# Kernel tuning notes

Measured on AMD Instinct MI355X. Metric: run time of the kernel, lower is better.

The kernel has to match this reference:

```python
import jax, jax.numpy as jnp
import numpy as np

B, Himg, Wimg, C = 4, 32, 32, 512
NUM_HEADS = 8
HEAD_DIM = C // NUM_HEADS          # 64
S_PATCH, L_PATCH = 4, 32           # key/value patch, query patch (l_patch == H so q has 1 patch)
SCALE = HEAD_DIM ** -0.5           # original code's self.scale is unset (bug); standard intent


def patchify(a, H, W, p):
    # a: [B, nh, N, hd] with N == H*W  ->  [B, nh, (H//p)*(W//p), p*p, hd]
    b, nh, n, hd = a.shape
    a = a.reshape(b, nh, H // p, p, W // p, p, hd)
    a = a.transpose(0, 1, 2, 4, 3, 5, 6)
    return a.reshape(b, nh, (H // p) * (W // p), p * p, hd)


def setup_inputs() -> dict:
    key = jax.random.key(0)
    ks = jax.random.split(key, 8)
    w_std = C ** -0.5  # keep qk logits O(1) so softmax is non-degenerate
    return {
        "x_s": jax.random.normal(ks[0], (B, Himg * Wimg, C), jnp.float32),
        "x_l": jax.random.normal(ks[1], (B, Himg * Wimg, C), jnp.float32),
        "Wq": jax.random.normal(ks[2], (C, C), jnp.float32) * w_std,
        "bq": jax.random.normal(ks[3], (C,), jnp.float32) * 0.01,
        "Wk": jax.random.normal(ks[4], (C, C), jnp.float32) * w_std,
        "bk": jax.random.normal(ks[5], (C,), jnp.float32) * 0.01,
        "Wv": jax.random.normal(ks[6], (C, C), jnp.float32) * w_std,
        "bv": jax.random.normal(ks[7], (C,), jnp.float32) * 0.01,
        "H": Himg,
        "W": Wimg,
    }


def reference(x_s, x_l, Wq, bq, Wk, bk, Wv, bv, H, W):
    b, n, c = x_s.shape
    # projections + split heads: [B, nh, N, hd]
    q = (x_l @ Wq + bq).reshape(b, n, NUM_HEADS, HEAD_DIM).transpose(0, 2, 1, 3)
    k = (x_s @ Wk + bk).reshape(b, n, NUM_HEADS, HEAD_DIM).transpose(0, 2, 1, 3)
    v = (x_s @ Wv + bv).reshape(b, n, NUM_HEADS, HEAD_DIM).transpose(0, 2, 1, 3)
    q_p = patchify(q, H, W, L_PATCH)   # [B, nh, 1,  L^2, hd]
    k_p = patchify(k, H, W, S_PATCH)   # [B, nh, Ps, s^2, hd]
    v_p = patchify(v, H, W, S_PATCH)   # [B, nh, Ps, s^2, hd]
    # broadcasted windowed cross-attention: [B, nh, Ps, L^2, s^2]
    attn = jnp.matmul(q_p, k_p.swapaxes(-2, -1)) * SCALE
    attn = jax.nn.softmax(attn, axis=-1)
    # dropout p=0.0 -> identity
    return jnp.matmul(attn, v_p)       # [B, nh, Ps, L^2, hd]
```

## Files before the change

### kernel.cpp

```cpp
#include <hip/hip_runtime.h>
#include <hip/hip_bf16.h>

#define NB 4
#define NH 8
#define NPX 1024
#define HD 64
#define CDIM 512
#define M_ROWS 4096
#define PS 64
#define S2 16

typedef __attribute__((ext_vector_type(8))) short bf16x8;
typedef __attribute__((ext_vector_type(4))) short bf16x4;
typedef __attribute__((ext_vector_type(4))) float f32x4;

typedef const __attribute__((address_space(1))) unsigned int* gptr_t;
typedef __attribute__((address_space(3))) unsigned int* lptr_t;

static __device__ __forceinline__ short f2bf(float f) {
    __hip_bfloat16 h = __float2bfloat16(f);
    return *reinterpret_cast<short*>(&h);
}

__global__ void convert_k(const float* __restrict__ xs, const float* __restrict__ xl,
                          const float* __restrict__ Wq, const float* __restrict__ Wk,
                          const float* __restrict__ Wv,
                          short* __restrict__ xl_bf, short* __restrict__ xs_bf,
                          short* __restrict__ WT ) {
    int i = blockIdx.x * blockDim.x + threadIdx.x;
    if (i < 524288) {
        float4 a = ((const float4*)xl)[i];
        float4 b = ((const float4*)xs)[i];
        short4 oa = make_short4(f2bf(a.x), f2bf(a.y), f2bf(a.z), f2bf(a.w));
        short4 ob = make_short4(f2bf(b.x), f2bf(b.y), f2bf(b.z), f2bf(b.w));
        ((short4*)xl_bf)[i] = oa;
        ((short4*)xs_bf)[i] = ob;
    }
    if (i < 786432) {
        int which = i >> 18;
        int j = i & 262143;
        int n = j >> 9, k = j & 511;
        const float* W = which == 0 ? Wq : (which == 1 ? Wk : Wv);
        WT[i] = f2bf(W[k * 512 + n]);
    }
}

__global__ __launch_bounds__(256, 3) void proj_gemm(
    const short* __restrict__ xl_bf, const short* __restrict__ xs_bf,
    const short* __restrict__ WT, const float* __restrict__ bq,
    const float* __restrict__ bk, const float* __restrict__ bv,
    short* __restrict__ qkv) {
    __shared__ __attribute__((aligned(16))) short A_lds[128 * 64];
    __shared__ __attribute__((aligned(16))) short B_lds[64 * 64];
    const int z = blockIdx.z;
    const int m0 = blockIdx.x * 128;
    const int n0 = blockIdx.y * 64;
    const short* A = (z == 0) ? xl_bf : xs_bf;
    const short* WTz = WT + z * 262144;
    const float* bias = (z == 0) ? bq : ((z == 1) ? bk : bv);
    short* out = qkv + (size_t)z * M_ROWS * CDIM;
    const int t = threadIdx.x, w = t >> 6, lane = t & 63;
    const int lr = lane & 15, g = lane >> 4;

    f32x4 acc[2][4] = {};
    for (int kt = 0; kt < 8; ++kt) {
        const int k0 = kt * 64;
#pragma unroll
        for (int r = 0; r < 4; ++r) {
            int c = r * 256 + t;
            int row = c >> 3, sub = c & 7;
            const short* src = A + (size_t)(m0 + row) * CDIM + k0 + ((sub ^ (row & 7)) * 8);
            __builtin_amdgcn_global_load_lds((gptr_t)src,
                (lptr_t)(A_lds + (r * 256 + w * 64) * 8), 16, 0, 0);
        }
#pragma unroll
        for (int r = 0; r < 2; ++r) {
            int c = r * 256 + t;
            int row = c >> 3, sub = c & 7;
            const short* src = WTz + (size_t)(n0 + row) * CDIM + k0 + ((sub ^ (row & 7)) * 8);
            __builtin_amdgcn_global_load_lds((gptr_t)src,
                (lptr_t)(B_lds + (r * 256 + w * 64) * 8), 16, 0, 0);
        }
        __syncthreads();
        bf16x8 afr[2][2], bfr[4][2];
#pragma unroll
        for (int mt = 0; mt < 2; ++mt)
#pragma unroll
            for (int kk = 0; kk < 2; ++kk) {
                int row = w * 32 + mt * 16 + lr;
                int slot = (kk * 4 + g) ^ (row & 7);
                afr[mt][kk] = *(const bf16x8*)(A_lds + row * 64 + slot * 8);
            }
#pragma unroll
        for (int nt = 0; nt < 4; ++nt)
#pragma unroll
            for (int kk = 0; kk < 2; ++kk) {
                int row = nt * 16 + lr;
                int slot = (kk * 4 + g) ^ (row & 7);
                bfr[nt][kk] = *(const bf16x8*)(B_lds + row * 64 + slot * 8);
            }
#pragma unroll
        for (int kk = 0; kk < 2; ++kk)
#pragma unroll
            for (int mt = 0; mt < 2; ++mt)
#pragma unroll
                for (int nt = 0; nt < 4; ++nt)
                    acc[mt][nt] = __builtin_amdgcn_mfma_f32_16x16x32_bf16(
                        afr[mt][kk], bfr[nt][kk], acc[mt][nt], 0, 0, 0);
        __syncthreads();
    }
#pragma unroll
    for (int mt = 0; mt < 2; ++mt) {
#pragma unroll
        for (int nt = 0; nt < 4; ++nt) {
            int col = n0 + nt * 16 + lr;
            float bv_ = bias[col];
            int row0 = m0 + w * 32 + mt * 16 + g * 4;
#pragma unroll
            for (int r = 0; r < 4; ++r)
                out[(size_t)(row0 + r) * CDIM + col] = f2bf(acc[mt][nt][r] + bv_);
        }
    }
}

__global__ void v_trans(const short* __restrict__ v_bf, short* __restrict__ vTp) {
    __shared__ __attribute__((aligned(16))) short lds[16 * 512];
    const int blk = blockIdx.x;
    const int b = blk >> 6, p = blk & 63;
    const int py = p >> 3, px = p & 7;
    const int t = threadIdx.x;
#pragma unroll
    for (int r = 0; r < 4; ++r) {
        int ci = r * 256 + t;
        int s = ci >> 6, c8 = (ci & 63) * 8;
        int n = py * 128 + (s >> 2) * 32 + px * 4 + (s & 3);
        *(bf16x8*)(lds + s * 512 + c8) =
            *(const bf16x8*)(v_bf + (size_t)(b * NPX + n) * CDIM + c8);
    }
    __syncthreads();
    const int h = t >> 5, d0 = (t & 31) * 2;
#pragma unroll
    for (int dd = 0; dd < 2; ++dd) {
        int d = d0 + dd;
        short tmp[16];
#pragma unroll
        for (int s = 0; s < 16; ++s) tmp[s] = lds[s * 512 + h * 64 + d];
        short* dst = vTp + ((size_t)((b * 8 + h) * PS + p) * HD + d) * S2;
        *(bf16x8*)(dst) = *(const bf16x8*)(tmp);
        *(bf16x8*)(dst + 8) = *(const bf16x8*)(tmp + 8);
    }
}

__global__ __launch_bounds__(256, 4) void attn_k(
    const short* __restrict__ q_bf, const short* __restrict__ k_bf,
    const short* __restrict__ vTp, float* __restrict__ out) {
    __shared__ __attribute__((aligned(16))) short k_lds[2][2][S2 * 64];
    __shared__ __attribute__((aligned(16))) float st_lds[4 * 16 * 68];
    const int bid = blockIdx.x;
    const int wid = ((bid & 7) << 7) | (bid >> 3);
    const int bh = wid >> 5;
    const int b = bh >> 3, h = bh & 7;
    const int rem = wid & 31;
    const int qtile = rem >> 1, pg = rem & 1;
    const int t = threadIdx.x, w = t >> 6, lane = t & 63;
    const int lr = lane & 15, g = lane >> 4;
    const int l_loc = qtile * 64 + w * 16 + lr;

    bf16x8 qfr[2];
    {
        const short* qrow = q_bf + (size_t)(b * NPX + l_loc) * CDIM + h * HD;
        qfr[0] = *(const bf16x8*)(qrow + g * 8);
        qfr[1] = *(const bf16x8*)(qrow + 32 + g * 8);
    }
    float* outbh = out + (size_t)bh * PS * NPX * HD;
    const int p0 = pg * 32;
    float* stw = st_lds + w * 1088;
    const int srow = lane >> 4, schunk = lane & 15;
    const short* vbase = vTp + ((size_t)(bh * PS) * HD + lr) * S2 + g * 4;

    const int s = t >> 4, c4 = (t & 15) * 4;
    const int swidx = (s * 64 + c4) ^ ((s & 7) << 3);
    const size_t rowbase = (size_t)(b * NPX) * CDIM + h * HD + c4;
    auto nidx = [&](int p) {
        int py = p >> 3, px = p & 7;
        return py * 128 + (s >> 2) * 32 + px * 4 + (s & 3);
    };
    short4 kreg[2];
    auto loadg = [&](int gi) {
#pragma unroll
        for (int pp = 0; pp < 2; ++pp) {
            int n = nidx(p0 + gi * 2 + pp);
            kreg[pp] = *(const short4*)(k_bf + rowbase + (size_t)n * CDIM);
        }
    };
    auto writeg = [&](int buf) {
#pragma unroll
        for (int pp = 0; pp < 2; ++pp)
            *(short4*)(&k_lds[buf][pp][swidx]) = kreg[pp];
    };
    loadg(0);
    writeg(0);
    for (int si = 0; si < 16; ++si) {
        const int buf = si & 1;
        asm volatile("s_waitcnt lgkmcnt(0)" ::: "memory");
        __builtin_amdgcn_s_barrier();
        __builtin_amdgcn_sched_barrier(0);
        if (si < 15) loadg(si + 1);
#pragma unroll
        for (int pp = 0; pp < 2; ++pp) {
            const int p = p0 + si * 2 + pp;
            const short* kb = k_lds[buf][pp];
            bf16x8 kfr0 = *(const bf16x8*)(kb + ((lr * 64 + g * 8) ^ ((lr & 7) << 3)));
            bf16x8 kfr1 = *(const bf16x8*)(kb + ((lr * 64 + 32 + g * 8) ^ ((lr & 7) << 3)));
            const short* vr = vbase + (size_t)p * HD * S2;
            bf16x4 vfr4[4];
#pragma unroll
            for (int dt = 0; dt < 4; ++dt)
                vfr4[dt] = *(const bf16x4*)(vr + dt * 16 * S2);

            f32x4 s_acc = {};
            s_acc = __builtin_amdgcn_mfma_f32_16x16x32_bf16(kfr0, qfr[0], s_acc, 0, 0, 0);
            s_acc = __builtin_amdgcn_mfma_f32_16x16x32_bf16(kfr1, qfr[1], s_acc, 0, 0, 0);
            float sv[4];
            float m = -1e30f;
#pragma unroll
            for (int r = 0; r < 4; ++r) { sv[r] = s_acc[r] * 0.125f; m = fmaxf(m, sv[r]); }
            m = fmaxf(m, __shfl_xor(m, 16));
            m = fmaxf(m, __shfl_xor(m, 32));
            float pv[4]; float sum = 0.f;
#pragma unroll
            for (int r = 0; r < 4; ++r) { pv[r] = __expf(sv[r] - m); sum += pv[r]; }
            sum += __shfl_xor(sum, 16);
            sum += __shfl_xor(sum, 32);
            float rs = 1.f / sum;
            bf16x8 pfr = { f2bf(pv[0] * rs), f2bf(pv[1] * rs), f2bf(pv[2] * rs), f2bf(pv[3] * rs),
                           0, 0, 0, 0 };
            f32x4 oacc[4];
#pragma unroll
            for (int dt = 0; dt < 4; ++dt) {
                bf16x8 vfr = { vfr4[dt][0], vfr4[dt][1], vfr4[dt][2], vfr4[dt][3], 0, 0, 0, 0 };
                f32x4 zero = {};
                oacc[dt] = __builtin_amdgcn_mfma_f32_16x16x32_bf16(vfr, pfr, zero, 0, 0, 0);
            }
#pragma unroll
            for (int dt = 0; dt < 4; ++dt)
                *(f32x4*)(stw + lr * 68 + dt * 16 + g * 4) = oacc[dt];
            float* opbase = outbh + ((size_t)p * NPX + qtile * 64 + w * 16) * HD;
#pragma unroll
            for (int u = 0; u < 4; ++u) {
                f32x4 vout = *(const f32x4*)(stw + (u * 4 + srow) * 68 + schunk * 4);
                *(f32x4*)(opbase + (size_t)(u * 4 + srow) * HD + schunk * 4) = vout;
            }
        }
        if (si < 15) writeg(buf ^ 1);
    }
}

extern "C" void kernel_launch(void* const* d_in, const int* in_sizes, int n_in,
                              void* d_out, int out_size, void* d_ws, size_t ws_size,
                              hipStream_t stream) {
    const float* x_s = (const float*)d_in[0];
    const float* x_l = (const float*)d_in[1];
    const float* Wq  = (const float*)d_in[2];
    const float* bq  = (const float*)d_in[3];
    const float* Wk  = (const float*)d_in[4];
    const float* bk  = (const float*)d_in[5];
    const float* Wv  = (const float*)d_in[6];
    const float* bv  = (const float*)d_in[7];
    float* out = (float*)d_out;
    char* ws = (char*)d_ws;

    short* xl_bf = (short*)(ws);
    short* xs_bf = (short*)(ws + 4194304);
    short* WT    = (short*)(ws + 8388608);
    short* qkv   = (short*)(ws + 9961472);
    short* q_bf = qkv;
    short* k_bf = qkv + 2097152;
    short* v_bf = qkv + 4194304;
    short* vTp  = (short*)(ws + 22544384);

    convert_k<<<3072, 256, 0, stream>>>(x_s, x_l, Wq, Wk, Wv, xl_bf, xs_bf, WT);
    proj_gemm<<<dim3(32, 8, 3), 256, 0, stream>>>(xl_bf, xs_bf, WT, bq, bk, bv, qkv);
    v_trans<<<256, 256, 0, stream>>>(v_bf, vTp);
    attn_k<<<1024, 256, 0, stream>>>(q_bf, k_bf, vTp, out);
}
```

Before: 138.3 us.

## Stage K and V tiles into LDS with async global_load_lds

Replaces the register-staged K loads with direct global-to-LDS async loads, and also stages V patches into double-buffered LDS instead of reading them from global inside the compute loop. The swizzle moves from the LDS write address to the global source column. Synchronisation becomes a vmcnt-based wait before the barrier at the end of each step. This removes VGPR round trips and scattered per-lane V global reads from the critical path. The cost is extra LDS, and correctness depends on the vmcnt counting with the interleaved output stores.

After: 138.6 us. About the same (+0.2%).

```diff
diff --git a/kernel.cpp b/kernel.cpp
--- a/kernel.cpp
+++ b/kernel.cpp
@@ -155,6 +155,7 @@
     const short* __restrict__ q_bf, const short* __restrict__ k_bf,
     const short* __restrict__ vTp, float* __restrict__ out) {
     __shared__ __attribute__((aligned(16))) short k_lds[2][2][S2 * 64];
+    __shared__ __attribute__((aligned(16))) short v_lds[2][2][HD * S2];
     __shared__ __attribute__((aligned(16))) float st_lds[4 * 16 * 68];
     const int bid = blockIdx.x;
     const int wid = ((bid & 7) << 7) | (bid >> 3);
@@ -176,47 +177,45 @@
     const int p0 = pg * 32;
     float* stw = st_lds + w * 1088;
     const int srow = lane >> 4, schunk = lane & 15;
-    const short* vbase = vTp + ((size_t)(bh * PS) * HD + lr) * S2 + g * 4;
-
-    const int s = t >> 4, c4 = (t & 15) * 4;
-    const int swidx = (s * 64 + c4) ^ ((s & 7) << 3);
-    const size_t rowbase = (size_t)(b * NPX) * CDIM + h * HD + c4;
-    auto nidx = [&](int p) {
+
+    const int spp = w >> 1;
+    const int cid = ((w & 1) << 6) | lane;
+    const int ks = cid >> 3, kc = cid & 7;
+    const size_t kbase = (size_t)(b * NPX) * CDIM + h * HD;
+    const short* vppbase = vTp + (size_t)(bh * PS) * HD * S2;
+    short* kdst = &k_lds[0][spp][(w & 1) * 512];
+    short* vdst = &v_lds[0][spp][(w & 1) * 512];
+    const int kcol = (kc ^ (ks & 7)) * 8;
+
+    auto stage = [&](int gi, int buf) {
+        int p = p0 + gi * 2 + spp;
         int py = p >> 3, px = p & 7;
-        return py * 128 + (s >> 2) * 32 + px * 4 + (s & 3);
+        int n = py * 128 + (ks >> 2) * 32 + px * 4 + (ks & 3);
+        const short* ksrc = k_bf + kbase + (size_t)n * CDIM + kcol;
+        __builtin_amdgcn_global_load_lds((gptr_t)ksrc,
+            (lptr_t)(kdst + buf * 2048), 16, 0, 0);
+        const short* vsrc = vppbase + (size_t)p * (HD * S2) + cid * 8;
+        __builtin_amdgcn_global_load_lds((gptr_t)vsrc,
+            (lptr_t)(vdst + buf * 2048), 16, 0, 0);
     };
-    short4 kreg[2];
-    auto loadg = [&](int gi) {
-#pragma unroll
-        for (int pp = 0; pp < 2; ++pp) {
-            int n = nidx(p0 + gi * 2 + pp);
-            kreg[pp] = *(const short4*)(k_bf + rowbase + (size_t)n * CDIM);
-        }
-    };
-    auto writeg = [&](int buf) {
-#pragma unroll
-        for (int pp = 0; pp < 2; ++pp)
-            *(short4*)(&k_lds[buf][pp][swidx]) = kreg[pp];
-    };
-    loadg(0);
-    writeg(0);
+    stage(0, 0);
+    asm volatile("s_waitcnt vmcnt(0)" ::: "memory");
+    __syncthreads();
+
     for (int si = 0; si < 16; ++si) {
         const int buf = si & 1;
-        asm volatile("s_waitcnt lgkmcnt(0)" ::: "memory");
-        __builtin_amdgcn_s_barrier();
-        __builtin_amdgcn_sched_barrier(0);
-        if (si < 15) loadg(si + 1);
+        if (si < 15) stage(si + 1, buf ^ 1);
 #pragma unroll
         for (int pp = 0; pp < 2; ++pp) {
             const int p = p0 + si * 2 + pp;
             const short* kb = k_lds[buf][pp];
             bf16x8 kfr0 = *(const bf16x8*)(kb + ((lr * 64 + g * 8) ^ ((lr & 7) << 3)));
             bf16x8 kfr1 = *(const bf16x8*)(kb + ((lr * 64 + 32 + g * 8) ^ ((lr & 7) << 3)));
-            const short* vr = vbase + (size_t)p * HD * S2;
+            const short* vb = v_lds[buf][pp];
             bf16x4 vfr4[4];
 #pragma unroll
             for (int dt = 0; dt < 4; ++dt)
-                vfr4[dt] = *(const bf16x4*)(vr + dt * 16 * S2);
+                vfr4[dt] = *(const bf16x4*)(vb + (dt * 16 + lr) * S2 + g * 4);
 
             f32x4 s_acc = {};
             s_acc = __builtin_amdgcn_mfma_f32_16x16x32_bf16(kfr0, qfr[0], s_acc, 0, 0, 0);
@@ -252,7 +251,11 @@
                 *(f32x4*)(opbase + (size_t)(u * 4 + srow) * HD + schunk * 4) = vout;
             }
         }
-        if (si < 15) writeg(buf ^ 1);
+        if (si < 15) {
+            asm volatile("s_waitcnt vmcnt(8) lgkmcnt(0)" ::: "memory");
+            __builtin_amdgcn_s_barrier();
+            __builtin_amdgcn_sched_barrier(0);
+        }
     }
 }
 
```
